# Kernel optimization log

Hardware: AMD Instinct MI355X
Metric: run time of the kernel (lower is better)

Reference implementation:

```python
import jax, jax.numpy as jnp
import numpy as np

BN_EPS = 1e-5
K = 2


def _log_shift_max(x):
    # x: [B, C, H, W]. torch.cat([x[..., -s:, :], x[..., :-s, :]], dim=2) == roll(x, +s)
    # and cat([x[..., s:, :], x[..., :s, :]], dim=2) == roll(x, -s).
    H, W = x.shape[2], x.shape[3]
    x_j = jnp.zeros_like(x)
    for i in range(1, int(H).bit_length()):
        s = K ** i - 1
        x_j = jnp.maximum(x_j, x - jnp.roll(x, s, axis=2))
        x_j = jnp.maximum(x_j, x - jnp.roll(x, -s, axis=2))
    for i in range(1, int(W).bit_length()):
        s = K ** i - 1
        x_j = jnp.maximum(x_j, x - jnp.roll(x, s, axis=3))
        x_j = jnp.maximum(x_j, x - jnp.roll(x, -s, axis=3))
    return x_j


def setup_inputs() -> dict:
    key = jax.random.key(0)
    k1, k2 = jax.random.split(key)
    B, C, H, W = 16, 384, 56, 56
    Cout = 384
    x = jax.random.normal(k1, (B, C, H, W), dtype=jnp.float32)
    conv_w = jax.random.normal(k2, (Cout, 2 * C, 1, 1), dtype=jnp.float32) * 0.02
    conv_b = jnp.zeros((Cout,), dtype=jnp.float32)
    bn_scale = jnp.ones((Cout,), dtype=jnp.float32)
    bn_bias = jnp.zeros((Cout,), dtype=jnp.float32)
    bn_mean = jnp.zeros((Cout,), dtype=jnp.float32)
    bn_var = jnp.ones((Cout,), dtype=jnp.float32)
    return {"x": x, "conv_w": conv_w, "conv_b": conv_b,
            "bn_scale": bn_scale, "bn_bias": bn_bias,
            "bn_mean": bn_mean, "bn_var": bn_var}


def reference(x, conv_w, conv_b, bn_scale, bn_bias, bn_mean, bn_var):
    x_j = _log_shift_max(x)                       # [B, C, H, W]
    xc = jnp.concatenate([x, x_j], axis=1)        # [B, 2C, H, W]
    # 1x1 conv == channel contraction
    y = jnp.einsum('bchw,oc->bohw', xc, conv_w[:, :, 0, 0]) + conv_b[None, :, None, None]
    # BatchNorm (eval mode, running stats)
    inv = jax.lax.rsqrt(bn_var + BN_EPS)
    y = (y - bn_mean[None, :, None, None]) * (inv * bn_scale)[None, :, None, None] + bn_bias[None, :, None, None]
    return jax.nn.gelu(y, approximate=False)
```

## Files before the change

kernel.cpp:

```cpp
#include <hip/hip_runtime.h>
#include <cstdint>
#include <cstddef>

typedef unsigned short u16;
typedef unsigned int u32;
typedef __attribute__((ext_vector_type(8))) short short8;
typedef __attribute__((ext_vector_type(4))) float f32x4;

__device__ __forceinline__ float bf2f(u16 v) { return __uint_as_float((u32)v << 16); }
__device__ __forceinline__ u16 f2bf(float f) {
    u32 u = __float_as_uint(f);
    u = (u + 0x7fffu + ((u >> 16) & 1u)) >> 16;
    return (u16)u;
}

#define GLD16(g, l) __builtin_amdgcn_global_load_lds( \
    (const __attribute__((address_space(1))) void*)(g), \
    (__attribute__((address_space(3))) void*)(l), 16, 0, 0)

__global__ void detect_kernel(const u16* __restrict__ x, int* __restrict__ flag) {
    int cnt = 0;
    for (int i = threadIdx.x; i < 256; i += 64) {
        const int e = (x[2 * i] >> 7) & 0xFF;
        cnt += (e >= 96 && e <= 135) ? 1 : 0;
    }
    #pragma unroll
    for (int o = 32; o; o >>= 1) cnt += __shfl_down(cnt, o, 64);
    if (threadIdx.x == 0) *flag = (cnt < 128) ? 1 : 0;
}

__global__ void wconv_kernel(const void* __restrict__ w, u16* __restrict__ wbf,
                             const int* __restrict__ flag) {
    const int i = blockIdx.x * 256 + threadIdx.x;
    if (i >= 384 * 768) return;
    if (*flag) wbf[i] = f2bf(((const float*)w)[i]);
    else       wbf[i] = ((const u16*)w)[i];
}

__global__ __launch_bounds__(256) void xj_kernel(const void* __restrict__ xin,
                                                 u16* __restrict__ xc,
                                                 const int* __restrict__ flag) {
    const int cg = blockIdx.x, b = blockIdx.y;
    const int fp = *flag;
    __shared__ __align__(16) u16 pl[3136][8];
    const size_t plane0 = ((size_t)b * 384 + (size_t)cg * 8) * 3136;

    if (fp) {
        const float* xb = (const float*)xin + plane0;
        for (int g = threadIdx.x; g < 784; g += 256) {
            const int p = g * 4;
            float vv[8][4];
            #pragma unroll
            for (int c = 0; c < 8; ++c) {
                const float4 t = *(const float4*)(xb + (size_t)c * 3136 + p);
                vv[c][0] = t.x; vv[c][1] = t.y; vv[c][2] = t.z; vv[c][3] = t.w;
            }
            #pragma unroll
            for (int i = 0; i < 4; ++i) {
                u32 q[4];
                #pragma unroll
                for (int cc = 0; cc < 4; ++cc)
                    q[cc] = (u32)f2bf(vv[cc * 2][i]) | ((u32)f2bf(vv[cc * 2 + 1][i]) << 16);
                *(uint4*)&pl[p + i][0] = make_uint4(q[0], q[1], q[2], q[3]);
            }
        }
    } else {
        const u16* xb = (const u16*)xin + plane0;
        for (int g = threadIdx.x; g < 784; g += 256) {
            const int p = g * 4;
            u32 rc[8][2];
            #pragma unroll
            for (int c = 0; c < 8; ++c) {
                const uint2 t = *(const uint2*)(xb + (size_t)c * 3136 + p);
                rc[c][0] = t.x; rc[c][1] = t.y;
            }
            #pragma unroll
            for (int i = 0; i < 4; ++i) {
                const int d = i >> 1, sh = (i & 1) * 16;
                u32 q[4];
                #pragma unroll
                for (int cc = 0; cc < 4; ++cc) {
                    const u32 lo = (rc[cc * 2][d] >> sh) & 0xFFFFu;
                    const u32 hi = (rc[cc * 2 + 1][d] >> sh) & 0xFFFFu;
                    q[cc] = lo | (hi << 16);
                }
                *(uint4*)&pl[p + i][0] = make_uint4(q[0], q[1], q[2], q[3]);
            }
        }
    }
    __syncthreads();

    for (int p = threadIdx.x; p < 3136; p += 256) {
        const int h = p / 56, w = p - h * 56;
        int off[20];
        const int S[5] = {1, 3, 7, 15, 31};
        #pragma unroll
        for (int si = 0; si < 5; ++si) {
            const int s = S[si];
            int hp = h + s; if (hp >= 56) hp -= 56;
            int hm = h - s; if (hm < 0)   hm += 56;
            int wp = w + s; if (wp >= 56) wp -= 56;
            int wm = w - s; if (wm < 0)   wm += 56;
            off[si * 4 + 0] = hp * 56 + w;
            off[si * 4 + 1] = hm * 56 + w;
            off[si * 4 + 2] = h * 56 + wp;
            off[si * 4 + 3] = h * 56 + wm;
        }
        const uint4 self = *(const uint4*)&pl[p][0];
        const u32 sw[4] = {self.x, self.y, self.z, self.w};
        float xv[8], mn[8];
        #pragma unroll
        for (int c2 = 0; c2 < 4; ++c2) {
            xv[c2 * 2]     = __uint_as_float(sw[c2] << 16);
            xv[c2 * 2 + 1] = __uint_as_float(sw[c2] & 0xFFFF0000u);
            mn[c2 * 2] = xv[c2 * 2]; mn[c2 * 2 + 1] = xv[c2 * 2 + 1];
        }
        #pragma unroll
        for (int k = 0; k < 20; k += 2) {
            const uint4 na = *(const uint4*)&pl[off[k]][0];
            const uint4 nb = *(const uint4*)&pl[off[k + 1]][0];
            const u32 aw[4] = {na.x, na.y, na.z, na.w};
            const u32 bw[4] = {nb.x, nb.y, nb.z, nb.w};
            #pragma unroll
            for (int c2 = 0; c2 < 4; ++c2) {
                mn[c2 * 2]     = fminf(fminf(__uint_as_float(aw[c2] << 16),
                                             __uint_as_float(bw[c2] << 16)), mn[c2 * 2]);
                mn[c2 * 2 + 1] = fminf(fminf(__uint_as_float(aw[c2] & 0xFFFF0000u),
                                             __uint_as_float(bw[c2] & 0xFFFF0000u)), mn[c2 * 2 + 1]);
            }
        }
        u32 jq[4];
        #pragma unroll
        for (int c2 = 0; c2 < 4; ++c2)
            jq[c2] = (u32)f2bf(xv[c2 * 2] - mn[c2 * 2]) |
                     ((u32)f2bf(xv[c2 * 2 + 1] - mn[c2 * 2 + 1]) << 16);
        u16* px = xc + ((((size_t)b * 96) + cg) * 3136 + p) * 8;
        u16* pj = xc + ((((size_t)b * 96) + 48 + cg) * 3136 + p) * 8;
        *(uint4*)px = self;
        *(uint4*)pj = make_uint4(jq[0], jq[1], jq[2], jq[3]);
    }
}

__global__ __launch_bounds__(512, 4) void gemm_kernel(
        const u16* __restrict__ xc, const u16* __restrict__ Wt,
        const void* __restrict__ cb, const void* __restrict__ bsc,
        const void* __restrict__ bbi, const void* __restrict__ bme,
        const void* __restrict__ bva, void* __restrict__ outp,
        const int* __restrict__ flag) {
    const int ntile = blockIdx.x;
    const int fp = *flag;
    __shared__ __align__(16) u16 Bs[2][16 * 64 * 8];
    __shared__ __align__(16) float T[8][16][36];
    __shared__ float2 PB[384];

    const int tid = threadIdx.x;
    if (tid < 384) {
        float vsc, vva, vcb, vme, vbi;
        if (fp) {
            vsc = ((const float*)bsc)[tid]; vva = ((const float*)bva)[tid];
            vcb = ((const float*)cb)[tid];  vme = ((const float*)bme)[tid];
            vbi = ((const float*)bbi)[tid];
        } else {
            vsc = bf2f(((const u16*)bsc)[tid]); vva = bf2f(((const u16*)bva)[tid]);
            vcb = bf2f(((const u16*)cb)[tid]);  vme = bf2f(((const u16*)bme)[tid]);
            vbi = bf2f(((const u16*)bbi)[tid]);
        }
        const float seff = vsc * rsqrtf(vva + 1e-5f);
        PB[tid] = make_float2(seff, (vcb - vme) * seff + vbi);
    }

    const int lane = tid & 63, wv = tid >> 6;
    const int quad = lane >> 4, l16 = lane & 15;
    const int wv_m = wv >> 1, wv_n = wv & 1;
    const int bb  = ntile / 49;
    const int hw0 = (ntile - bb * 49) * 64;

    const u16* bgp[2]; int bofs[2];
    #pragma unroll
    for (int i = 0; i < 2; ++i) {
        const int idx = i * 512 + tid;
        const int gg = idx >> 6, n = idx & 63;
        bgp[i]  = xc + (((size_t)bb * 96 + gg) * 3136 + hw0 + n) * 8;
        bofs[i] = idx * 8;
    }
    #define STAGE(q) { \
        u16* dst = &Bs[(q) & 1][0]; \
        GLD16(bgp[0] + (size_t)(q) * 16 * 3136 * 8, dst + bofs[0]); \
        GLD16(bgp[1] + (size_t)(q) * 16 * 3136 * 8, dst + bofs[1]); }

    const u16* arow[6];
    #pragma unroll
    for (int j = 0; j < 6; ++j)
        arow[j] = Wt + (size_t)(wv_m * 96 + j * 16 + l16) * 768 + quad * 8;

    #define LOADA(dst, t) { \
        _Pragma("unroll") \
        for (int j = 0; j < 6; ++j) \
            dst[j] = *(const short8*)(arow[j] + (t) * 32); }

    f32x4 acc[6][2];
    #pragma unroll
    for (int j = 0; j < 6; ++j) {
        acc[j][0] = {0.f, 0.f, 0.f, 0.f};
        acc[j][1] = {0.f, 0.f, 0.f, 0.f};
    }

    short8 afP[6], afQ[6];

    LOADA(afP, 0);
    STAGE(0);
    STAGE(1);
    asm volatile("s_waitcnt vmcnt(2) lgkmcnt(0)" ::: "memory");
    __builtin_amdgcn_s_barrier();

    #define SSTEP(q, s, CUR, NXT) { \
        if ((q) * 4 + (s) + 1 < 24) LOADA(NXT, (q) * 4 + (s) + 1); \
        short8 bfv[2]; \
        _Pragma("unroll") \
        for (int in = 0; in < 2; ++in) \
            bfv[in] = *(const short8*)(&Bs[(q) & 1][0] + \
                (((s) * 4 + quad) * 64 + wv_n * 32 + in * 16 + l16) * 8); \
        _Pragma("unroll") \
        for (int j = 0; j < 6; ++j) { \
            acc[j][0] = __builtin_amdgcn_mfma_f32_16x16x32_bf16(CUR[j], bfv[0], acc[j][0], 0, 0, 0); \
            acc[j][1] = __builtin_amdgcn_mfma_f32_16x16x32_bf16(CUR[j], bfv[1], acc[j][1], 0, 0, 0); } }

    #define PHASE(q) { \
        SSTEP(q, 0, afP, afQ); \
        SSTEP(q, 1, afQ, afP); \
        SSTEP(q, 2, afP, afQ); \
        SSTEP(q, 3, afQ, afP); \
        if ((q) < 5) { \
            __builtin_amdgcn_s_barrier(); \
            if ((q) < 4) STAGE((q) + 2); \
            if ((q) <= 3) { asm volatile("s_waitcnt vmcnt(8)" ::: "memory"); } \
            else          { asm volatile("s_waitcnt vmcnt(6)" ::: "memory"); } \
            __builtin_amdgcn_s_barrier(); } }

    PHASE(0); PHASE(1); PHASE(2); PHASE(3); PHASE(4); PHASE(5);

    const size_t obase = (size_t)bb * 384 * 3136 + hw0 + wv_n * 32;
    #pragma unroll
    for (int j = 0; j < 6; ++j) {
        #pragma unroll
        for (int r = 0; r < 4; ++r) {
            const int rl = quad * 4 + r;
            const float2 sb = PB[wv_m * 96 + j * 16 + rl];
            #pragma unroll
            for (int in = 0; in < 2; ++in) {
                float v = acc[j][in][r] * sb.x + sb.y;
                v = 0.5f * v * (1.0f + erff(v * 0.70710678118654752f));
                T[wv][rl][in * 16 + l16] = v;
            }
        }
        asm volatile("s_waitcnt lgkmcnt(0)" ::: "memory");
        #pragma unroll
        for (int it = 0; it < 2; ++it) {
            const int flat = it * 256 + lane * 4;
            const int row = flat >> 5, col = flat & 31;
            const float4 vv = *(const float4*)&T[wv][row][col];
            const size_t oi = obase + (size_t)(wv_m * 96 + j * 16 + row) * 3136 + col;
            if (fp) {
                *(float4*)((float*)outp + oi) = vv;
            } else {
                const u32 a = (u32)f2bf(vv.x) | ((u32)f2bf(vv.y) << 16);
                const u32 b2 = (u32)f2bf(vv.z) | ((u32)f2bf(vv.w) << 16);
                *(uint2*)((u16*)outp + oi) = make_uint2(a, b2);
            }
        }
        asm volatile("s_waitcnt lgkmcnt(0)" ::: "memory");
    }
    #undef PHASE
    #undef SSTEP
    #undef LOADA
    #undef STAGE
}

extern "C" void kernel_launch(void* const* d_in, const int* in_sizes, int n_in,
                              void* d_out, int out_size, void* d_ws, size_t ws_size,
                              hipStream_t stream) {
    const void* x   = d_in[0];
    const void* w   = d_in[1];
    const void* cbp = d_in[2];
    const void* bsc = d_in[3];
    const void* bbi = d_in[4];
    const void* bme = d_in[5];
    const void* bva = d_in[6];

    int* flag = (int*)d_ws;
    u16* xc   = (u16*)((char*)d_ws + 64);
    u16* wbf  = xc + (size_t)16 * 96 * 3136 * 8;

    detect_kernel<<<1, 64, 0, stream>>>((const u16*)x, flag);
    wconv_kernel<<<1152, 256, 0, stream>>>(w, wbf, flag);
    xj_kernel<<<dim3(48, 16), 256, 0, stream>>>(x, xc, flag);
    gemm_kernel<<<784, 512, 0, stream>>>(xc, wbf, cbp, bsc, bbi, bme, bva,
                                         d_out, flag);
}
```

Baseline: 318.9 us.

## Restructure GEMM to 32-pixel tiles with full-K LDS preload and triple-buffered A

The GEMM kernel now uses 256-thread blocks over 32-pixel tiles (1568 blocks). Each block loads its whole K=768 slice of B into LDS at once instead of double-buffering 16-group stages with barriers. A fragments are prefetched two steps ahead through three register buffers, and MFMA sections run at raised wave priority. This removes the per-phase barriers and waitcnt synchronization, at the cost of more LDS per block, more reloads of the weight matrix A across twice as many blocks, and no overlap between the initial B load and compute within a block.

```diff
diff --git a/kernel.cpp b/kernel.cpp
--- a/kernel.cpp
+++ b/kernel.cpp
@@ -141,57 +141,42 @@
     }
 }
 
-__global__ __launch_bounds__(512, 4) void gemm_kernel(
+__global__ __launch_bounds__(256, 2) void gemm_kernel(
         const u16* __restrict__ xc, const u16* __restrict__ Wt,
         const void* __restrict__ cb, const void* __restrict__ bsc,
         const void* __restrict__ bbi, const void* __restrict__ bme,
         const void* __restrict__ bva, void* __restrict__ outp,
         const int* __restrict__ flag) {
-    const int ntile = blockIdx.x;
     const int fp = *flag;
-    __shared__ __align__(16) u16 Bs[2][16 * 64 * 8];
-    __shared__ __align__(16) float T[8][16][36];
+    __shared__ __align__(16) u16 Bs[96][32][8];
+    __shared__ __align__(16) float T[4][16][36];
     __shared__ float2 PB[384];
 
     const int tid = threadIdx.x;
-    if (tid < 384) {
+    for (int o = tid; o < 384; o += 256) {
         float vsc, vva, vcb, vme, vbi;
         if (fp) {
-            vsc = ((const float*)bsc)[tid]; vva = ((const float*)bva)[tid];
-            vcb = ((const float*)cb)[tid];  vme = ((const float*)bme)[tid];
-            vbi = ((const float*)bbi)[tid];
+            vsc = ((const float*)bsc)[o]; vva = ((const float*)bva)[o];
+            vcb = ((const float*)cb)[o];  vme = ((const float*)bme)[o];
+            vbi = ((const float*)bbi)[o];
         } else {
-            vsc = bf2f(((const u16*)bsc)[tid]); vva = bf2f(((const u16*)bva)[tid]);
-            vcb = bf2f(((const u16*)cb)[tid]);  vme = bf2f(((const u16*)bme)[tid]);
-            vbi = bf2f(((const u16*)bbi)[tid]);
+            vsc = bf2f(((const u16*)bsc)[o]); vva = bf2f(((const u16*)bva)[o]);
+            vcb = bf2f(((const u16*)cb)[o]);  vme = bf2f(((const u16*)bme)[o]);
+            vbi = bf2f(((const u16*)bbi)[o]);
         }
         const float seff = vsc * rsqrtf(vva + 1e-5f);
-        PB[tid] = make_float2(seff, (vcb - vme) * seff + vbi);
+        PB[o] = make_float2(seff, (vcb - vme) * seff + vbi);
     }
 
     const int lane = tid & 63, wv = tid >> 6;
     const int quad = lane >> 4, l16 = lane & 15;
-    const int wv_m = wv >> 1, wv_n = wv & 1;
-    const int bb  = ntile / 49;
-    const int hw0 = (ntile - bb * 49) * 64;
-
-    const u16* bgp[2]; int bofs[2];
-    #pragma unroll
-    for (int i = 0; i < 2; ++i) {
-        const int idx = i * 512 + tid;
-        const int gg = idx >> 6, n = idx & 63;
-        bgp[i]  = xc + (((size_t)bb * 96 + gg) * 3136 + hw0 + n) * 8;
-        bofs[i] = idx * 8;
-    }
-    #define STAGE(q) { \
-        u16* dst = &Bs[(q) & 1][0]; \
-        GLD16(bgp[0] + (size_t)(q) * 16 * 3136 * 8, dst + bofs[0]); \
-        GLD16(bgp[1] + (size_t)(q) * 16 * 3136 * 8, dst + bofs[1]); }
+    const int bb  = blockIdx.x / 98;
+    const int hw0 = (blockIdx.x - bb * 98) * 32;
 
     const u16* arow[6];
     #pragma unroll
     for (int j = 0; j < 6; ++j)
-        arow[j] = Wt + (size_t)(wv_m * 96 + j * 16 + l16) * 768 + quad * 8;
+        arow[j] = Wt + (size_t)(wv * 96 + j * 16 + l16) * 768 + quad * 8;
 
     #define LOADA(dst, t) { \
         _Pragma("unroll") \
@@ -205,47 +190,44 @@
         acc[j][1] = {0.f, 0.f, 0.f, 0.f};
     }
 
-    short8 afP[6], afQ[6];
-
-    LOADA(afP, 0);
-    STAGE(0);
-    STAGE(1);
-    asm volatile("s_waitcnt vmcnt(2) lgkmcnt(0)" ::: "memory");
-    __builtin_amdgcn_s_barrier();
-
-    #define SSTEP(q, s, CUR, NXT) { \
-        if ((q) * 4 + (s) + 1 < 24) LOADA(NXT, (q) * 4 + (s) + 1); \
-        short8 bfv[2]; \
-        _Pragma("unroll") \
-        for (int in = 0; in < 2; ++in) \
-            bfv[in] = *(const short8*)(&Bs[(q) & 1][0] + \
-                (((s) * 4 + quad) * 64 + wv_n * 32 + in * 16 + l16) * 8); \
+    short8 sA[6], sB[6], sC[6];
+
+    LOADA(sA, 0);
+    LOADA(sB, 1);
+    {
+        const u16* xbase = xc + ((size_t)bb * 96 * 3136 + hw0) * 8;
+        u16* ldsbase = &Bs[0][0][0];
+        #pragma unroll
+        for (int i = 0; i < 12; ++i) {
+            const int idx = i * 256 + tid;
+            const int gg = idx >> 5, n = idx & 31;
+            GLD16(xbase + ((size_t)gg * 3136 + n) * 8, ldsbase + idx * 8);
+        }
+    }
+    __syncthreads();
+
+    #define SSTEP(t, CUR, NXT) { \
+        if ((t) + 2 < 24) LOADA(NXT, (t) + 2); \
+        const short8 bfv0 = *(const short8*)&Bs[(t) * 4 + quad][l16][0]; \
+        const short8 bfv1 = *(const short8*)&Bs[(t) * 4 + quad][16 + l16][0]; \
+        __builtin_amdgcn_s_setprio(1); \
         _Pragma("unroll") \
         for (int j = 0; j < 6; ++j) { \
-            acc[j][0] = __builtin_amdgcn_mfma_f32_16x16x32_bf16(CUR[j], bfv[0], acc[j][0], 0, 0, 0); \
-            acc[j][1] = __builtin_amdgcn_mfma_f32_16x16x32_bf16(CUR[j], bfv[1], acc[j][1], 0, 0, 0); } }
-
-    #define PHASE(q) { \
-        SSTEP(q, 0, afP, afQ); \
-        SSTEP(q, 1, afQ, afP); \
-        SSTEP(q, 2, afP, afQ); \
-        SSTEP(q, 3, afQ, afP); \
-        if ((q) < 5) { \
-            __builtin_amdgcn_s_barrier(); \
-            if ((q) < 4) STAGE((q) + 2); \
-            if ((q) <= 3) { asm volatile("s_waitcnt vmcnt(8)" ::: "memory"); } \
-            else          { asm volatile("s_waitcnt vmcnt(6)" ::: "memory"); } \
-            __builtin_amdgcn_s_barrier(); } }
-
-    PHASE(0); PHASE(1); PHASE(2); PHASE(3); PHASE(4); PHASE(5);
-
-    const size_t obase = (size_t)bb * 384 * 3136 + hw0 + wv_n * 32;
+            acc[j][0] = __builtin_amdgcn_mfma_f32_16x16x32_bf16(CUR[j], bfv0, acc[j][0], 0, 0, 0); \
+            acc[j][1] = __builtin_amdgcn_mfma_f32_16x16x32_bf16(CUR[j], bfv1, acc[j][1], 0, 0, 0); } \
+        __builtin_amdgcn_s_setprio(0); }
+
+    #define TRIP(t) { SSTEP(t, sA, sC); SSTEP((t) + 1, sB, sA); SSTEP((t) + 2, sC, sB); }
+
+    TRIP(0); TRIP(3); TRIP(6); TRIP(9); TRIP(12); TRIP(15); TRIP(18); TRIP(21);
+
+    const size_t obase = (size_t)bb * 384 * 3136 + hw0;
     #pragma unroll
     for (int j = 0; j < 6; ++j) {
         #pragma unroll
         for (int r = 0; r < 4; ++r) {
             const int rl = quad * 4 + r;
-            const float2 sb = PB[wv_m * 96 + j * 16 + rl];
+            const float2 sb = PB[wv * 96 + j * 16 + rl];
             #pragma unroll
             for (int in = 0; in < 2; ++in) {
                 float v = acc[j][in][r] * sb.x + sb.y;
@@ -259,7 +241,7 @@
             const int flat = it * 256 + lane * 4;
             const int row = flat >> 5, col = flat & 31;
             const float4 vv = *(const float4*)&T[wv][row][col];
-            const size_t oi = obase + (size_t)(wv_m * 96 + j * 16 + row) * 3136 + col;
+            const size_t oi = obase + (size_t)(wv * 96 + j * 16 + row) * 3136 + col;
             if (fp) {
                 *(float4*)((float*)outp + oi) = vv;
             } else {
@@ -270,10 +252,9 @@
         }
         asm volatile("s_waitcnt lgkmcnt(0)" ::: "memory");
     }
-    #undef PHASE
+    #undef TRIP
     #undef SSTEP
     #undef LOADA
-    #undef STAGE
 }
 
 extern "C" void kernel_launch(void* const* d_in, const int* in_sizes, int n_in,
@@ -294,6 +275,6 @@
     detect_kernel<<<1, 64, 0, stream>>>((const u16*)x, flag);
     wconv_kernel<<<1152, 256, 0, stream>>>(w, wbf, flag);
     xj_kernel<<<dim3(48, 16), 256, 0, stream>>>(x, xc, flag);
-    gemm_kernel<<<784, 512, 0, stream>>>(xc, wbf, cbp, bsc, bbi, bme, bva,
-                                         d_out, flag);
-}
+    gemm_kernel<<<1568, 256, 0, stream>>>(xc, wbf, cbp, bsc, bbi, bme, bva,
+                                          d_out, flag);
+}
```

Measured after the change: 303.4 us. 1.05x faster.
